# Performance work log

Hardware: AMD Instinct MI355X
Metric: run time of the kernel (lower is better)

The kernel has to match this reference:

```python
import jax, jax.numpy as jnp
import numpy as np

B, N, F_IN = 32, 1024, 128
H1, H2, OUT = 64, 32, 10
EDGE_P = 0.01  # edge probability for random adjacency


def setup_inputs() -> dict:
    key = jax.random.key(0)
    ks = jax.random.split(key, 16)
    x = jax.random.normal(ks[0], (B, N, F_IN), dtype=jnp.float32)
    # dense binary adjacency per graph (module consumes dense [N,N] adj)
    adj = (jax.random.uniform(ks[1], (B, N, N)) < EDGE_P).astype(jnp.float32)
    mask = jnp.ones((B, N, 1), dtype=jnp.float32)
    s = 0.05
    W1a = jax.random.normal(ks[2], (F_IN, H1), dtype=jnp.float32) * s
    b1a = jnp.zeros((H1,), dtype=jnp.float32)
    W2a = jax.random.normal(ks[3], (H1, H1), dtype=jnp.float32) * s
    b2a = jnp.zeros((H1,), dtype=jnp.float32)
    W1b = jax.random.normal(ks[4], (H1, H2), dtype=jnp.float32) * s
    b1b = jnp.zeros((H2,), dtype=jnp.float32)
    W2b = jax.random.normal(ks[5], (H2, H2), dtype=jnp.float32) * s
    b2b = jnp.zeros((H2,), dtype=jnp.float32)
    Wfc = jax.random.normal(ks[6], (H2, OUT), dtype=jnp.float32) * s
    bfc = jnp.zeros((OUT,), dtype=jnp.float32)
    return dict(x=x, adj=adj, mask=mask, W1a=W1a, b1a=b1a, W2a=W2a, b2a=b2a,
                W1b=W1b, b1b=b1b, W2b=W2b, b2b=b2b, Wfc=Wfc, bfc=bfc)


def _gin_layer(h, adj, mask, Wa, ba, Wb, bb, eps=0.0):
    # neighbor sum aggregation: neigh[b,i] = sum_j adj[b,i,j] * h[b,j]
    neigh = jnp.einsum('bij,bjf->bif', adj, h)
    z = (1.0 + eps) * h + neigh
    z = jax.nn.relu(z @ Wa + ba) @ Wb + bb  # 2-layer MLP
    return z * mask  # zero out padded nodes


def reference(x, adj, mask, W1a, b1a, W2a, b2a, W1b, b1b, W2b, b2b, Wfc, bfc):
    h = _gin_layer(x, adj, mask, W1a, b1a, W2a, b2a)   # [B,N,64]
    h = _gin_layer(h, adj, mask, W1b, b1b, W2b, b2b)   # [B,N,32]
    g = jnp.max(h, axis=1)                              # graph readout [B,32]
    return g @ Wfc + bfc                                # [B,OUT] (dropout = eval identity)
```

## Files before the change

### kernel.cpp

```cpp
#include <hip/hip_runtime.h>
#include <cstdint>
#include <cstddef>


#define CAP 64

typedef float v4f __attribute__((ext_vector_type(4)));

__device__ __forceinline__ float rl(float x, int l) {
  return __int_as_float(__builtin_amdgcn_readlane(__float_as_int(x), l));
}

__global__ __launch_bounds__(256) void k_scanproj(
    const float* __restrict__ x, const float* __restrict__ W1a,
    float* __restrict__ u,
    const float* __restrict__ adj, int* __restrict__ nbr,
    int* __restrict__ deg) {
  int lane = threadIdx.x & 63;
  int wid  = threadIdx.x >> 6;
  if (blockIdx.x < 1024) {
    int row0 = (blockIdx.x * 4 + wid) * 8;
    row0 = __builtin_amdgcn_readfirstlane(row0);
    const float* xr = x + (size_t)row0 * 128;
    float acc[8] = {0, 0, 0, 0, 0, 0, 0, 0};
    for (int kc = 0; kc < 32; ++kc) {
      v4f xv[8];
      #pragma unroll
      for (int r = 0; r < 8; ++r)
        xv[r] = *(const v4f*)(xr + r * 128 + kc * 4);
      #pragma unroll
      for (int j = 0; j < 4; ++j) {
        float w = W1a[(kc * 4 + j) * 64 + lane];
        #pragma unroll
        for (int r = 0; r < 8; ++r)
          acc[r] = fmaf(xv[r][j], w, acc[r]);
      }
    }
    #pragma unroll
    for (int r = 0; r < 8; ++r)
      u[(size_t)(row0 + r) * 64 + lane] = acc[r];
  } else {
    int node = (blockIdx.x - 1024) * 4 + wid;
    const v4f* arow = (const v4f*)(adj + (size_t)node * 1024);
    int* outp = nbr + node * CAP;
    v4f a[4];
    #pragma unroll
    for (int c = 0; c < 4; ++c)
      a[c] = __builtin_nontemporal_load(arow + c * 64 + lane);
    int cnt = 0;
    #pragma unroll
    for (int c = 0; c < 4; ++c) {
      #pragma unroll
      for (int comp = 0; comp < 4; ++comp) {
        bool hit = (a[c][comp] != 0.0f);
        unsigned long long m = __ballot(hit);
        if (hit) {
          int below = __builtin_amdgcn_mbcnt_hi(
              (unsigned)(m >> 32),
              __builtin_amdgcn_mbcnt_lo((unsigned)m, 0));
          int pos = cnt + below;
          if (pos < CAP) outp[pos] = ((c * 64 + lane) << 2) + comp;
        }
        cnt += __popcll(m);
      }
    }
    if (lane == 0) deg[node] = cnt < CAP ? cnt : CAP;
  }
}

__global__ __launch_bounds__(256) void k_gathA(
    const float* __restrict__ u, const int* __restrict__ nbr,
    const int* __restrict__ deg, const float* __restrict__ mask,
    const float* __restrict__ b1a, const float* __restrict__ W2a,
    const float* __restrict__ b2a, const float* __restrict__ W1b,
    float* __restrict__ v) {
  __shared__ float sW2[64 * 64];
  __shared__ float sW1b[64 * 32];
  for (int t = threadIdx.x; t < 64 * 64; t += 256) sW2[t] = W2a[t];
  for (int t = threadIdx.x; t < 64 * 32; t += 256) sW1b[t] = W1b[t];
  __syncthreads();
  int lane = threadIdx.x & 63;
  int f = lane & 31, hh = lane >> 5;
  float ba1 = b1a[lane], ba2 = b2a[lane];
  int i = blockIdx.x, wid = threadIdx.x >> 6;
  int xcd = i & 7, j = i >> 3;
  int b = xcd + 8 * (j & 3);
  int w = j >> 2;
  int n0 = b * 1024 + w * 8 + wid * 2, n1 = n0 + 1;
  const float* ub = u + (size_t)b * 1024 * 64;
  int d0 = deg[n0], d1 = deg[n1];
  int nl0 = nbr[n0 * CAP + lane], nl1 = nbr[n1 * CAP + lane];
  float s0[8] = {0,0,0,0,0,0,0,0}, s1[8] = {0,0,0,0,0,0,0,0};
  int dmax = d0 > d1 ? d0 : d1;
  int rounds = (dmax + 7) >> 3;
  for (int rr = 0; rr < rounds; ++rr) {
    int base = rr << 3;
    #pragma unroll
    for (int i2 = 0; i2 < 8; ++i2) {
      int t = base + i2;
      int j0 = __builtin_amdgcn_readlane(nl0, t);
      int j1 = __builtin_amdgcn_readlane(nl1, t);
      bool ok0 = t < d0, ok1 = t < d1;
      j0 = ok0 ? j0 : 0;  j1 = ok1 ? j1 : 0;
      float v0 = ub[j0 * 64 + lane];
      float v1 = ub[j1 * 64 + lane];
      s0[i2] += ok0 ? v0 : 0.0f;
      s1[i2] += ok1 ? v1 : 0.0f;
    }
  }
  float acc0 = ub[(n0 & 1023) * 64 + lane]
             + (((s0[0]+s0[1])+(s0[2]+s0[3]))+((s0[4]+s0[5])+(s0[6]+s0[7])));
  float acc1 = ub[(n1 & 1023) * 64 + lane]
             + (((s1[0]+s1[1])+(s1[2]+s1[3]))+((s1[4]+s1[5])+(s1[6]+s1[7])));
  float r0 = fmaxf(acc0 + ba1, 0.0f);
  float r1 = fmaxf(acc1 + ba1, 0.0f);
  float a0=0,a1=0,a2=0,a3=0, c0=0,c1=0,c2=0,c3=0;
  #pragma unroll
  for (int k = 0; k < 64; k += 4) {
    float w0 = sW2[(k    ) * 64 + lane];
    float w1 = sW2[(k + 1) * 64 + lane];
    float w2 = sW2[(k + 2) * 64 + lane];
    float w3 = sW2[(k + 3) * 64 + lane];
    a0 = fmaf(rl(r0, k    ), w0, a0);  c0 = fmaf(rl(r1, k    ), w0, c0);
    a1 = fmaf(rl(r0, k + 1), w1, a1);  c1 = fmaf(rl(r1, k + 1), w1, c1);
    a2 = fmaf(rl(r0, k + 2), w2, a2);  c2 = fmaf(rl(r1, k + 2), w2, c2);
    a3 = fmaf(rl(r0, k + 3), w3, a3);  c3 = fmaf(rl(r1, k + 3), w3, c3);
  }
  float h20 = (ba2 + ((a0 + a1) + (a2 + a3))) * mask[n0];
  float h21 = (ba2 + ((c0 + c1) + (c2 + c3))) * mask[n1];
  float p00=0,p01=0, p10=0,p11=0;
  #pragma unroll
  for (int k0 = 0; k0 < 32; k0 += 2) {
    float w0 = sW1b[(hh * 32 + k0    ) * 32 + f];
    float w1 = sW1b[(hh * 32 + k0 + 1) * 32 + f];
    p00 = fmaf(__shfl(h20, hh * 32 + k0    ), w0, p00);
    p01 = fmaf(__shfl(h20, hh * 32 + k0 + 1), w1, p01);
    p10 = fmaf(__shfl(h21, hh * 32 + k0    ), w0, p10);
    p11 = fmaf(__shfl(h21, hh * 32 + k0 + 1), w1, p11);
  }
  float vp0 = p00 + p01;  vp0 += __shfl_xor(vp0, 32);
  float vp1 = p10 + p11;  vp1 += __shfl_xor(vp1, 32);
  if (hh == 0) {
    v[n0 * 32 + f] = vp0;
    v[n1 * 32 + f] = vp1;
  }
}

__global__ __launch_bounds__(256) void k_gathB(
    const float* __restrict__ v, const int* __restrict__ nbr,
    const int* __restrict__ deg, const float* __restrict__ mask,
    const float* __restrict__ b1b, const float* __restrict__ W2b,
    const float* __restrict__ b2b, float* __restrict__ pmax) {
  __shared__ float sW2b[32 * 32];
  __shared__ float wred[4][32];
  for (int t = threadIdx.x; t < 32 * 32; t += 256) sW2b[t] = W2b[t];
  __syncthreads();
  int lane = threadIdx.x & 63;
  int f = lane & 31, hh = lane >> 5;
  float bb1 = b1b[f], bb2 = b2b[f];
  int i = blockIdx.x, wid = threadIdx.x >> 6;
  int xcd = i & 7, j = i >> 3;
  int b = xcd + 8 * (j & 3);
  int w = j >> 2;
  int n0 = b * 1024 + w * 8 + wid * 2, n1 = n0 + 1;
  const float* vb = v + (size_t)b * 1024 * 32;
  int d0 = deg[n0], d1 = deg[n1];
  int nl0 = nbr[n0 * CAP + lane], nl1 = nbr[n1 * CAP + lane];
  float s0[8] = {0,0,0,0,0,0,0,0}, s1[8] = {0,0,0,0,0,0,0,0};
  int dmax = d0 > d1 ? d0 : d1;
  int rounds = (dmax + 15) >> 4;
  for (int rr = 0; rr < rounds; ++rr) {
    int base = rr << 4;
    #pragma unroll
    for (int i2 = 0; i2 < 8; ++i2) {
      int t = base + (i2 << 1) + hh;
      int j0 = __shfl(nl0, t);
      int j1 = __shfl(nl1, t);
      bool ok0 = t < d0, ok1 = t < d1;
      j0 = ok0 ? j0 : 0;  j1 = ok1 ? j1 : 0;
      float v0 = vb[j0 * 32 + f];
      float v1 = vb[j1 * 32 + f];
      s0[i2] += ok0 ? v0 : 0.0f;
      s1[i2] += ok1 ? v1 : 0.0f;
    }
  }
  float acc0 = ((s0[0]+s0[1])+(s0[2]+s0[3]))+((s0[4]+s0[5])+(s0[6]+s0[7]));
  float acc1 = ((s1[0]+s1[1])+(s1[2]+s1[3]))+((s1[4]+s1[5])+(s1[6]+s1[7]));
  acc0 += __shfl_xor(acc0, 32);
  acc1 += __shfl_xor(acc1, 32);
  float r0 = fmaxf(vb[(n0 & 1023) * 32 + f] + acc0 + bb1, 0.0f);
  float r1 = fmaxf(vb[(n1 & 1023) * 32 + f] + acc1 + bb1, 0.0f);
  float a0=0,a1=0,a2=0,a3=0, c0=0,c1=0,c2=0,c3=0;
  #pragma unroll
  for (int k = 0; k < 32; k += 4) {
    float w0 = sW2b[(k    ) * 32 + f];
    float w1 = sW2b[(k + 1) * 32 + f];
    float w2 = sW2b[(k + 2) * 32 + f];
    float w3 = sW2b[(k + 3) * 32 + f];
    a0 = fmaf(rl(r0, k    ), w0, a0);  c0 = fmaf(rl(r1, k    ), w0, c0);
    a1 = fmaf(rl(r0, k + 1), w1, a1);  c1 = fmaf(rl(r1, k + 1), w1, c1);
    a2 = fmaf(rl(r0, k + 2), w2, a2);  c2 = fmaf(rl(r1, k + 2), w2, c2);
    a3 = fmaf(rl(r0, k + 3), w3, a3);  c3 = fmaf(rl(r1, k + 3), w3, c3);
  }
  float o0 = (bb2 + ((a0 + a1) + (a2 + a3))) * mask[n0];
  float o1 = (bb2 + ((c0 + c1) + (c2 + c3))) * mask[n1];
  float m = fmaxf(o0, o1);
  if (hh == 0) wred[wid][f] = m;
  __syncthreads();
  if (threadIdx.x < 32) {
    float mm = fmaxf(fmaxf(wred[0][threadIdx.x], wred[1][threadIdx.x]),
                     fmaxf(wred[2][threadIdx.x], wred[3][threadIdx.x]));
    pmax[((b << 7) + w) * 32 + threadIdx.x] = mm;
  }
}

__global__ __launch_bounds__(1024) void k_fin(
    const float* __restrict__ pmax, const float* __restrict__ Wfc,
    const float* __restrict__ bfc, float* __restrict__ out) {
  __shared__ float red[32][33];
  __shared__ float g[32];
  int b = blockIdx.x;
  int f = threadIdx.x & 31, c = threadIdx.x >> 5;
  const float* pb = pmax + (size_t)b * 128 * 32;
  float m = -3.4e38f;
  #pragma unroll
  for (int q = 0; q < 4; ++q)
    m = fmaxf(m, pb[(c * 4 + q) * 32 + f]);
  red[c][f] = m;
  __syncthreads();
  if (c == 0) {
    float mm = red[0][f];
    #pragma unroll
    for (int k = 1; k < 32; ++k) mm = fmaxf(mm, red[k][f]);
    g[f] = mm;
  }
  __syncthreads();
  if (threadIdx.x < 10) {
    float o = bfc[threadIdx.x];
    #pragma unroll
    for (int k = 0; k < 32; ++k)
      o = fmaf(g[k], Wfc[k * 10 + threadIdx.x], o);
    out[b * 10 + threadIdx.x] = o;
  }
}

extern "C" void kernel_launch(void* const* d_in, const int* in_sizes, int n_in,
                              void* d_out, int out_size, void* d_ws, size_t ws_size,
                              hipStream_t stream) {
  const float* x    = (const float*)d_in[0];
  const float* adj  = (const float*)d_in[1];
  const float* mask = (const float*)d_in[2];
  const float* W1a  = (const float*)d_in[3];
  const float* b1a  = (const float*)d_in[4];
  const float* W2a  = (const float*)d_in[5];
  const float* b2a  = (const float*)d_in[6];
  const float* W1b  = (const float*)d_in[7];
  const float* b1b  = (const float*)d_in[8];
  const float* W2b  = (const float*)d_in[9];
  const float* b2b  = (const float*)d_in[10];
  const float* Wfc  = (const float*)d_in[11];
  const float* bfc  = (const float*)d_in[12];
  float* out = (float*)d_out;

  char* ws = (char*)d_ws;
  float* u    = (float*)(ws);
  float* v    = (float*)(ws + (8u << 20));
  int*   nbr  = (int*)  (ws + (12u << 20));
  int*   deg  = (int*)  (ws + (20u << 20));
  float* pmax = (float*)(ws + (21u << 20));

  hipLaunchKernelGGL(k_scanproj, dim3(9216), dim3(256),  0, stream,
                     x, W1a, u, adj, nbr, deg);
  hipLaunchKernelGGL(k_gathA,    dim3(4096), dim3(256),  0, stream,
                     u, nbr, deg, mask, b1a, W2a, b2a, W1b, v);
  hipLaunchKernelGGL(k_gathB,    dim3(4096), dim3(256),  0, stream,
                     v, nbr, deg, mask, b1b, W2b, b2b, pmax);
  hipLaunchKernelGGL(k_fin,      dim3(32),   dim3(1024), 0, stream,
                     pmax, Wfc, bfc, out);
}
```

Before: 275.2 us.

## Shrink neighbor lists to u16, overlap weight staging, atomic max readout

Neighbor indices are stored as 16-bit values, halving the neighbor-list traffic written by the scan and read by both gather kernels. In the gather kernels, weight loads into registers are issued before the neighbor gather and written to shared memory afterwards, overlapping weight-fetch latency with the gather. The per-block partial max buffer is replaced by an order-preserving uint atomicMax into a small per-graph array, zeroed by the first scan block. The final kernel then becomes a single small block. This adds atomics and relies on launch ordering for the zero-initialisation.

```diff
diff --git a/kernel.cpp b/kernel.cpp
--- a/kernel.cpp
+++ b/kernel.cpp
@@ -14,10 +14,14 @@
 __global__ __launch_bounds__(256) void k_scanproj(
     const float* __restrict__ x, const float* __restrict__ W1a,
     float* __restrict__ u,
-    const float* __restrict__ adj, int* __restrict__ nbr,
-    int* __restrict__ deg) {
+    const float* __restrict__ adj, unsigned short* __restrict__ nbr,
+    int* __restrict__ deg, unsigned* __restrict__ g_u32) {
   int lane = threadIdx.x & 63;
   int wid  = threadIdx.x >> 6;
+  if (blockIdx.x == 0) {
+    #pragma unroll
+    for (int i = 0; i < 4; ++i) g_u32[threadIdx.x * 4 + i] = 0u;
+  }
   if (blockIdx.x < 1024) {
     int row0 = (blockIdx.x * 4 + wid) * 8;
     row0 = __builtin_amdgcn_readfirstlane(row0);
@@ -42,7 +46,7 @@
   } else {
     int node = (blockIdx.x - 1024) * 4 + wid;
     const v4f* arow = (const v4f*)(adj + (size_t)node * 1024);
-    int* outp = nbr + node * CAP;
+    unsigned short* outp = nbr + node * CAP;
     v4f a[4];
     #pragma unroll
     for (int c = 0; c < 4; ++c)
@@ -59,7 +63,8 @@
               (unsigned)(m >> 32),
               __builtin_amdgcn_mbcnt_lo((unsigned)m, 0));
           int pos = cnt + below;
-          if (pos < CAP) outp[pos] = ((c * 64 + lane) << 2) + comp;
+          if (pos < CAP)
+            outp[pos] = (unsigned short)(((c * 64 + lane) << 2) + comp);
         }
         cnt += __popcll(m);
       }
@@ -69,16 +74,18 @@
 }
 
 __global__ __launch_bounds__(256) void k_gathA(
-    const float* __restrict__ u, const int* __restrict__ nbr,
+    const float* __restrict__ u, const unsigned short* __restrict__ nbr,
     const int* __restrict__ deg, const float* __restrict__ mask,
     const float* __restrict__ b1a, const float* __restrict__ W2a,
     const float* __restrict__ b2a, const float* __restrict__ W1b,
     float* __restrict__ v) {
   __shared__ float sW2[64 * 64];
   __shared__ float sW1b[64 * 32];
-  for (int t = threadIdx.x; t < 64 * 64; t += 256) sW2[t] = W2a[t];
-  for (int t = threadIdx.x; t < 64 * 32; t += 256) sW1b[t] = W1b[t];
-  __syncthreads();
+  float wr2[16], wr1[8];
+  #pragma unroll
+  for (int i = 0; i < 16; ++i) wr2[i] = W2a[threadIdx.x + i * 256];
+  #pragma unroll
+  for (int i = 0; i < 8; ++i)  wr1[i] = W1b[threadIdx.x + i * 256];
   int lane = threadIdx.x & 63;
   int f = lane & 31, hh = lane >> 5;
   float ba1 = b1a[lane], ba2 = b2a[lane];
@@ -112,6 +119,11 @@
              + (((s0[0]+s0[1])+(s0[2]+s0[3]))+((s0[4]+s0[5])+(s0[6]+s0[7])));
   float acc1 = ub[(n1 & 1023) * 64 + lane]
              + (((s1[0]+s1[1])+(s1[2]+s1[3]))+((s1[4]+s1[5])+(s1[6]+s1[7])));
+  #pragma unroll
+  for (int t = 0; t < 16; ++t) sW2[threadIdx.x + t * 256] = wr2[t];
+  #pragma unroll
+  for (int t = 0; t < 8; ++t)  sW1b[threadIdx.x + t * 256] = wr1[t];
+  __syncthreads();
   float r0 = fmaxf(acc0 + ba1, 0.0f);
   float r1 = fmaxf(acc1 + ba1, 0.0f);
   float a0=0,a1=0,a2=0,a3=0, c0=0,c1=0,c2=0,c3=0;
@@ -147,14 +159,15 @@
 }
 
 __global__ __launch_bounds__(256) void k_gathB(
-    const float* __restrict__ v, const int* __restrict__ nbr,
+    const float* __restrict__ v, const unsigned short* __restrict__ nbr,
     const int* __restrict__ deg, const float* __restrict__ mask,
     const float* __restrict__ b1b, const float* __restrict__ W2b,
-    const float* __restrict__ b2b, float* __restrict__ pmax) {
+    const float* __restrict__ b2b, unsigned* __restrict__ g_u32) {
   __shared__ float sW2b[32 * 32];
   __shared__ float wred[4][32];
-  for (int t = threadIdx.x; t < 32 * 32; t += 256) sW2b[t] = W2b[t];
-  __syncthreads();
+  float wrb[4];
+  #pragma unroll
+  for (int i = 0; i < 4; ++i) wrb[i] = W2b[threadIdx.x + i * 256];
   int lane = threadIdx.x & 63;
   int f = lane & 31, hh = lane >> 5;
   float bb1 = b1b[f], bb2 = b2b[f];
@@ -188,6 +201,9 @@
   float acc1 = ((s1[0]+s1[1])+(s1[2]+s1[3]))+((s1[4]+s1[5])+(s1[6]+s1[7]));
   acc0 += __shfl_xor(acc0, 32);
   acc1 += __shfl_xor(acc1, 32);
+  #pragma unroll
+  for (int t = 0; t < 4; ++t) sW2b[threadIdx.x + t * 256] = wrb[t];
+  __syncthreads();
   float r0 = fmaxf(vb[(n0 & 1023) * 32 + f] + acc0 + bb1, 0.0f);
   float r1 = fmaxf(vb[(n1 & 1023) * 32 + f] + acc1 + bb1, 0.0f);
   float a0=0,a1=0,a2=0,a3=0, c0=0,c1=0,c2=0,c3=0;
@@ -210,37 +226,33 @@
   if (threadIdx.x < 32) {
     float mm = fmaxf(fmaxf(wred[0][threadIdx.x], wred[1][threadIdx.x]),
                      fmaxf(wred[2][threadIdx.x], wred[3][threadIdx.x]));
-    pmax[((b << 7) + w) * 32 + threadIdx.x] = mm;
-  }
-}
-
-__global__ __launch_bounds__(1024) void k_fin(
-    const float* __restrict__ pmax, const float* __restrict__ Wfc,
+    unsigned bu  = __float_as_uint(mm);
+    unsigned key = bu ^ ((unsigned)((int)bu >> 31) | 0x80000000u);
+    atomicMax(&g_u32[(b << 5) + threadIdx.x], key);
+  }
+}
+
+__global__ __launch_bounds__(320) void k_fin(
+    const unsigned* __restrict__ g_u32, const float* __restrict__ Wfc,
     const float* __restrict__ bfc, float* __restrict__ out) {
-  __shared__ float red[32][33];
-  __shared__ float g[32];
-  int b = blockIdx.x;
-  int f = threadIdx.x & 31, c = threadIdx.x >> 5;
-  const float* pb = pmax + (size_t)b * 128 * 32;
-  float m = -3.4e38f;
-  #pragma unroll
-  for (int q = 0; q < 4; ++q)
-    m = fmaxf(m, pb[(c * 4 + q) * 32 + f]);
-  red[c][f] = m;
-  __syncthreads();
-  if (c == 0) {
-    float mm = red[0][f];
-    #pragma unroll
-    for (int k = 1; k < 32; ++k) mm = fmaxf(mm, red[k][f]);
-    g[f] = mm;
-  }
-  __syncthreads();
-  if (threadIdx.x < 10) {
-    float o = bfc[threadIdx.x];
+  __shared__ float g[1024];
+  int t = threadIdx.x;
+  if (t < 256) {
+    #pragma unroll
+    for (int i = 0; i < 4; ++i) {
+      unsigned key  = g_u32[t * 4 + i];
+      unsigned flip = (key >> 31) ? 0x80000000u : 0xFFFFFFFFu;
+      g[t * 4 + i] = __uint_as_float(key ^ flip);
+    }
+  }
+  __syncthreads();
+  int b = t / 10, o = t - b * 10;
+  if (b < 32) {
+    float acc = bfc[o];
     #pragma unroll
     for (int k = 0; k < 32; ++k)
-      o = fmaf(g[k], Wfc[k * 10 + threadIdx.x], o);
-    out[b * 10 + threadIdx.x] = o;
+      acc = fmaf(g[b * 32 + k], Wfc[k * 10 + o], acc);
+    out[b * 10 + o] = acc;
   }
 }
 
@@ -263,18 +275,18 @@
   float* out = (float*)d_out;
 
   char* ws = (char*)d_ws;
-  float* u    = (float*)(ws);
-  float* v    = (float*)(ws + (8u << 20));
-  int*   nbr  = (int*)  (ws + (12u << 20));
-  int*   deg  = (int*)  (ws + (20u << 20));
-  float* pmax = (float*)(ws + (21u << 20));
-
-  hipLaunchKernelGGL(k_scanproj, dim3(9216), dim3(256),  0, stream,
-                     x, W1a, u, adj, nbr, deg);
-  hipLaunchKernelGGL(k_gathA,    dim3(4096), dim3(256),  0, stream,
+  float*          u     = (float*)(ws);
+  float*          v     = (float*)(ws + (8u  << 20));
+  unsigned short* nbr   = (unsigned short*)(ws + (12u << 20));
+  int*            deg   = (int*)  (ws + (16u << 20));
+  unsigned*       g_u32 = (unsigned*)(ws + (17u << 20));
+
+  hipLaunchKernelGGL(k_scanproj, dim3(9216), dim3(256), 0, stream,
+                     x, W1a, u, adj, nbr, deg, g_u32);
+  hipLaunchKernelGGL(k_gathA,    dim3(4096), dim3(256), 0, stream,
                      u, nbr, deg, mask, b1a, W2a, b2a, W1b, v);
-  hipLaunchKernelGGL(k_gathB,    dim3(4096), dim3(256),  0, stream,
-                     v, nbr, deg, mask, b1b, W2b, b2b, pmax);
-  hipLaunchKernelGGL(k_fin,      dim3(32),   dim3(1024), 0, stream,
-                     pmax, Wfc, bfc, out);
-}
+  hipLaunchKernelGGL(k_gathB,    dim3(4096), dim3(256), 0, stream,
+                     v, nbr, deg, mask, b1b, W2b, b2b, g_u32);
+  hipLaunchKernelGGL(k_fin,      dim3(1),    dim3(320), 0, stream,
+                     g_u32, Wfc, bfc, out);
+}
```

After: 269.0 us. 2.3% less time.
